# Optimization experiments

Measured on AMD Instinct MI355X. Metric: run time of the kernel, lower is better.

## Reference

```python
import jax, jax.numpy as jnp
import numpy as np

LEVEL_N = [81920, 20480, 5120, 1280, 320]  # faces at div..div-4 (div=6, 20*4^d)
K = 10  # SpherePHD conv kernel taps
W_SHAPES = [(64,3),(64,64),(128,64),(128,128),(256,128),(256,256),(256,256),(512,256),(512,512),(512,512),(512,512),(512,512),(512,512)]
BLOCKS = [[0,1],[2,3],[4,5,6],[7,8,9],[10,11,12]]  # conv indices per VGG block


def setup_inputs() -> dict:
    key = jax.random.key(0)
    ks = iter(jax.random.split(key, 64))
    d = {"x": jax.random.normal(next(ks), (2, 3, LEVEL_N[0]), jnp.float32)}
    for l, n in enumerate(LEVEL_N):
        d[f"conv_t{l}"] = jax.random.randint(next(ks), (n, K), 0, n, jnp.int32)
        d[f"adj_t{l}"] = jax.random.randint(next(ks), (n, 4), 0, n, jnp.int32)
        d[f"pool_t{l}"] = jax.random.randint(next(ks), (n // 4,), 0, n, jnp.int32)
    for i, (o, c) in enumerate(W_SHAPES):
        d[f"w{i}"] = jax.random.normal(next(ks), (o, c, K), jnp.float32) * (1.0 / np.sqrt(c * K))
        d[f"b{i}"] = jnp.zeros((o,), jnp.float32)
    return d


def phd_conv(x, w, b, table):
    # x: [B,C,N], table: [N,K] -> gather neighbors [B,C,N,K], weighted sum, ReLU
    g = x[:, :, table]
    y = jnp.einsum('bcnk,ock->bon', g, w) + b[None, :, None]
    return jax.nn.relu(y)


def phd_maxpool(x, adj, pool):
    # max over adjacent faces, then subsample to parent faces
    m = jnp.max(x[:, :, adj], axis=-1)  # [B,C,N]
    return m[:, :, pool]                # [B,C,N/4]


def reference(x, conv_t0, conv_t1, conv_t2, conv_t3, conv_t4,
              adj_t0, adj_t1, adj_t2, adj_t3, adj_t4,
              pool_t0, pool_t1, pool_t2, pool_t3, pool_t4,
              w0, w1, w2, w3, w4, w5, w6, w7, w8, w9, w10, w11, w12,
              b0, b1, b2, b3, b4, b5, b6, b7, b8, b9, b10, b11, b12):
    conv_ts = [conv_t0, conv_t1, conv_t2, conv_t3, conv_t4]
    adj_ts = [adj_t0, adj_t1, adj_t2, adj_t3, adj_t4]
    pool_ts = [pool_t0, pool_t1, pool_t2, pool_t3, pool_t4]
    ws = [w0, w1, w2, w3, w4, w5, w6, w7, w8, w9, w10, w11, w12]
    bs = [b0, b1, b2, b3, b4, b5, b6, b7, b8, b9, b10, b11, b12]
    h = x
    for lvl, idxs in enumerate(BLOCKS):
        for i in idxs:
            h = phd_conv(h, ws[i], bs[i], conv_ts[lvl])
        h = phd_maxpool(h, adj_ts[lvl], pool_ts[lvl])
    return h  # [2, 512, 80]
```

## Files before the change

### kernel.cpp

```cpp
#include <hip/hip_runtime.h>
#include <stdint.h>

typedef __bf16 bf16;
typedef bf16 bf16x8 __attribute__((ext_vector_type(8)));
typedef float f32x4 __attribute__((ext_vector_type(4)));
typedef unsigned short u16x8 __attribute__((ext_vector_type(8)));

__device__ __forceinline__ void gload_lds16(const bf16* g, bf16* l) {
    __builtin_amdgcn_global_load_lds(
        (const __attribute__((address_space(1))) void*)g,
        (__attribute__((address_space(3))) void*)l, 16, 0, 0);
}

struct PrepArgs {
    const float* src[12];
    int base[12];
    int dstoff[12];
    int Clog[12];
    int OT[12];
    int nClog[12];
};

__global__ __launch_bounds__(256) void prep_frag(PrepArgs a, bf16* __restrict__ dst)
{
    __shared__ bf16 lds[16 * 648];
    int bid = blockIdx.x;
    int l = 0;
#pragma unroll
    for (int i = 1; i < 12; i++) if (bid >= a.base[i]) l = i;
    int local = bid - a.base[l];
    int nClog = a.nClog[l];
    int cchunk = local & ((1 << nClog) - 1);
    int ot = local >> nClog;
    int Clog = a.Clog[l];
    int CK10 = 10 << Clog;
    const float* src = a.src[l];
    int t = threadIdx.x;

    size_t sbase = (size_t)(ot * 16) * CK10 + (size_t)cchunk * 640;
#pragma unroll
    for (int it = 0; it < 10; it++) {
        int idx = t + it * 256;
        int m = idx / 160;
        int i4 = idx - m * 160;
        float4 v = *(const float4*)(src + sbase + (size_t)m * CK10 + i4 * 4);
        bf16 b4[4] = {(bf16)v.x, (bf16)v.y, (bf16)v.z, (bf16)v.w};
        *(ushort4*)(&lds[m * 648 + i4 * 4]) = *(ushort4*)b4;
    }
    __syncthreads();

    int sub = t >> 6, ll = t & 63;
    int m = ll & 15, q = ll >> 4;
    int OTl = a.OT[l];
    size_t dbase = (size_t)a.dstoff[l];
#pragma unroll
    for (int tt = 0; tt < 5; tt++) {
        int tile = sub + tt * 4;
        int k = tile >> 1, half = tile & 1;
        int k32 = (k << (Clog - 5)) + cchunk * 2 + half;
        bf16 tmp[8];
#pragma unroll
        for (int j = 0; j < 8; j++)
            tmp[j] = lds[m * 648 + (half * 32 + q * 8 + j) * 10 + k];
        *(bf16x8*)(dst + dbase + ((size_t)(k32 * OTl + ot) << 9) + ll * 8) =
            *(bf16x8*)tmp;
    }
}

__global__ __launch_bounds__(256) void conv0_kernel(
    const float* __restrict__ x, const float* __restrict__ w0,
    const float* __restrict__ b0, const int* __restrict__ table,
    bf16* __restrict__ out)
{
    const int N = 81920;
    __shared__ float wls[30][64];
    __shared__ float bls[64];
    int tid = threadIdx.x;
    for (int i = tid; i < 1920; i += 256) {
        int o = i / 30, ck = i - o * 30;
        wls[ck][o] = w0[i];
    }
    if (tid < 64) bls[tid] = b0[tid];
    __syncthreads();

    int p = blockIdx.x * 256 + tid;
    int b = p >= N;
    int n = p - b * N;
    int idx[10];
    const int* trow = table + n * 10;
#pragma unroll
    for (int k = 0; k < 10; k++) idx[k] = trow[k];
    float xv[30];
#pragma unroll
    for (int c = 0; c < 3; c++)
#pragma unroll
        for (int k = 0; k < 10; k++)
            xv[c * 10 + k] = x[(b * 3 + c) * N + idx[k]];

    float acc[64];
#pragma unroll
    for (int o = 0; o < 64; o++) acc[o] = bls[o];
    for (int ck = 0; ck < 30; ck++) {
        float xs = xv[ck];
        const f32x4* wrow = (const f32x4*)(&wls[ck][0]);
#pragma unroll
        for (int o4 = 0; o4 < 16; o4++) {
            f32x4 w4 = wrow[o4];
            acc[o4 * 4 + 0] += xs * w4[0];
            acc[o4 * 4 + 1] += xs * w4[1];
            acc[o4 * 4 + 2] += xs * w4[2];
            acc[o4 * 4 + 3] += xs * w4[3];
        }
    }
    bf16x8 ob[8];
#pragma unroll
    for (int i = 0; i < 8; i++)
#pragma unroll
        for (int e = 0; e < 8; e++)
            ob[i][e] = (bf16)fmaxf(acc[i * 8 + e], 0.0f);
    bf16x8* dst = (bf16x8*)(out + (size_t)p * 64);
#pragma unroll
    for (int i = 0; i < 8; i++) dst[i] = ob[i];
}

template<int C, int TO, int TP>
__global__ __launch_bounds__(256) void conv_f(
    const bf16* __restrict__ in, const bf16* __restrict__ wfrag,
    const float* __restrict__ bias, const int* __restrict__ table,
    bf16* __restrict__ out, float* __restrict__ slab,
    int N, int O, int S, int PO)
{
    constexpr int BP = TP * 32;
    constexpr int CH = C / 64;
    constexpr int CHUNKS = CH * 10;
    constexpr int NW = 2 * TO + TP;
    constexpr int IMM = NW | 0x70 | 0xF00;
    __shared__ bf16 Xs[3][BP][64];
    __shared__ int rowoff[BP][10];

    const int tid = threadIdx.x;
    const int lane = tid & 63;
    const int wid = tid >> 6;
    const int wo = wid & 1, wp = wid >> 1;
    const int l16 = lane & 15, q = lane >> 4;

    const int p0 = blockIdx.x * BP;
    const int o0 = blockIdx.y * (TO * 32);
    const int z = blockIdx.z;
    const int OT = O >> 4;

    for (int j = tid; j < BP * 10; j += 256) {
        int pp = j / 10, k = j - pp * 10;
        int p = p0 + pp;
        int b = p >= N;
        int n = p - b * N;
        rowoff[pp][k] = (b * N + table[n * 10 + k]) * C;
    }
    __syncthreads();

    const int lrow = lane >> 3;
    const int gs = (lane & 7) ^ lrow;
    int srow[TP];
#pragma unroll
    for (int t = 0; t < TP; t++) srow[t] = wid * (TP * 8) + t * 8 + lrow;

    const int obase = (o0 >> 4) + wo * TO;

    const int per = CHUNKS / S;
    const int ck0 = z * per;

    auto stage = [&](int chunk, int b3) {
        int k = chunk / CH;
        int cofs = (chunk & (CH - 1)) * 64;
#pragma unroll
        for (int t = 0; t < TP; t++)
            gload_lds16(in + rowoff[srow[t]][k] + cofs + gs * 8,
                        &Xs[b3][wid * (TP * 8) + t * 8][0]);
    };
    auto loadW = [&](int chunk, bf16x8* dstA) {
        int k32b = chunk * 2;
#pragma unroll
        for (int ks = 0; ks < 2; ks++)
#pragma unroll
            for (int to = 0; to < TO; to++)
                dstA[ks * TO + to] = *(const bf16x8*)(
                    wfrag + (((size_t)(k32b + ks) * OT + obase + to) << 9) + lane * 8);
    };

    f32x4 acc[TO][TP];
#pragma unroll
    for (int a = 0; a < TO; a++)
#pragma unroll
        for (int c = 0; c < TP; c++) acc[a][c] = (f32x4){0.f, 0.f, 0.f, 0.f};

    bf16x8 wrA[2 * TO], wrB[2 * TO];

    stage(ck0, 0);
    loadW(ck0, wrA);
    stage(ck0 + 1, 1);

    const int browb = wp * (TP * 16);
    const int sx = l16 & 7;

    auto iter = [&](int j, bf16x8* cur, bf16x8* nxt, int bi, int bs) {
        __builtin_amdgcn_s_waitcnt(IMM);
        __builtin_amdgcn_s_barrier();
        __builtin_amdgcn_sched_barrier(0);
        int wc = j + 1 < per ? j + 1 : per - 1;
        loadW(ck0 + wc, nxt);
        int xc = j + 2 < per ? j + 2 : per - 1;
        stage(ck0 + xc, bs);
        __builtin_amdgcn_sched_barrier(0);
        const bf16* xb = &Xs[bi][0][0];
#pragma unroll
        for (int ks = 0; ks < 2; ks++) {
            int slot = ((ks * 4 + q) ^ sx) * 8;
            bf16x8 bfr[TP];
#pragma unroll
            for (int tp = 0; tp < TP; tp++)
                bfr[tp] = *(const bf16x8*)(xb + (browb + tp * 16 + l16) * 64 + slot);
#pragma unroll
            for (int to = 0; to < TO; to++)
#pragma unroll
                for (int tp = 0; tp < TP; tp++)
                    acc[to][tp] = __builtin_amdgcn_mfma_f32_16x16x32_bf16(
                        cur[ks * TO + to], bfr[tp], acc[to][tp], 0, 0, 0);
        }
    };

    int bi = 0, bs = 2;
    for (int j = 0; j < per; j += 2) {
        iter(j, wrA, wrB, bi, bs);
        bi = bi == 2 ? 0 : bi + 1; bs = bs == 2 ? 0 : bs + 1;
        iter(j + 1, wrB, wrA, bi, bs);
        bi = bi == 2 ? 0 : bi + 1; bs = bs == 2 ? 0 : bs + 1;
    }

    if (S == 1) {
#pragma unroll
        for (int to = 0; to < TO; ++to) {
            int ob = o0 + wo * (TO * 16) + to * 16 + q * 4;
            f32x4 bv = *(const f32x4*)(bias + ob);
#pragma unroll
            for (int tp = 0; tp < TP; ++tp) {
                int p = p0 + browb + tp * 16 + l16;
                union { ushort4 u4; unsigned short s[4]; } pk;
#pragma unroll
                for (int r = 0; r < 4; r++) {
                    float v = fmaxf(acc[to][tp][r] + bv[r], 0.0f);
                    union { bf16 h; unsigned short u; } cc;
                    cc.h = (bf16)v;
                    pk.s[r] = cc.u;
                }
                *(ushort4*)(out + (size_t)p * O + ob) = pk.u4;
            }
        }
    } else {
        float* sb = slab + (size_t)z * PO;
#pragma unroll
        for (int to = 0; to < TO; ++to) {
            int ob = o0 + wo * (TO * 16) + to * 16 + q * 4;
#pragma unroll
            for (int tp = 0; tp < TP; ++tp) {
                int p = p0 + browb + tp * 16 + l16;
                __builtin_nontemporal_store(acc[to][tp],
                    (f32x4*)(sb + (size_t)p * O + ob));
            }
        }
    }
}

__global__ __launch_bounds__(256) void epi_reduce(
    const float* __restrict__ slab, const float* __restrict__ bias,
    bf16* __restrict__ out, int PO, int Omask, int S)
{
    int t4 = (blockIdx.x * 256 + threadIdx.x) * 4;
    if (t4 >= PO) return;
    f32x4 s = __builtin_nontemporal_load((const f32x4*)(slab + t4));
    for (int zz = 1; zz < S; zz++)
        s += __builtin_nontemporal_load((const f32x4*)(slab + (size_t)zz * PO + t4));
    int o = t4 & Omask;
    f32x4 bv = *(const f32x4*)(bias + o);
    union { ushort4 u4; unsigned short e[4]; } pk;
#pragma unroll
    for (int r = 0; r < 4; r++) {
        float v = fmaxf(s[r] + bv[r], 0.0f);
        union { bf16 h; unsigned short u; } cc;
        cc.h = (bf16)v;
        pk.e[r] = cc.u;
    }
    *(ushort4*)((unsigned short*)out + t4) = pk.u4;
}

__global__ __launch_bounds__(256) void pool_kernel(
    const bf16* __restrict__ in, const int* __restrict__ adj,
    const int* __restrict__ pool, bf16* __restrict__ out,
    int N, int M, int c8shift)
{
    int t = blockIdx.x * 256 + threadIdx.x;
    int total = M << c8shift;
    if (t >= total) return;
    int cc = t & ((1 << c8shift) - 1);
    int j = t >> c8shift;
    int b = blockIdx.y;
    int C = 8 << c8shift;
    int s = pool[j];
    const int* a = adj + s * 4;
    const unsigned short* inu = (const unsigned short*)in;
    size_t base = (size_t)b * N * C + (size_t)cc * 8;
    u16x8 m = *(const u16x8*)(inu + base + (size_t)a[0] * C);
#pragma unroll
    for (int i = 1; i < 4; i++) {
        u16x8 v = *(const u16x8*)(inu + base + (size_t)a[i] * C);
#pragma unroll
        for (int e = 0; e < 8; e++) m[e] = v[e] > m[e] ? v[e] : m[e];
    }
    *(u16x8*)((unsigned short*)out + ((size_t)b * M + j) * C + (size_t)cc * 8) = m;
}

__global__ __launch_bounds__(256) void final_pool(
    const bf16* __restrict__ in, const int* __restrict__ adj,
    const int* __restrict__ pool, float* __restrict__ out)
{
    int t = blockIdx.x * 256 + threadIdx.x;
    if (t >= 81920) return;
    int j = t % 80;
    int rest = t / 80;
    int c = rest & 511;
    int b = rest >> 9;
    int s = pool[j];
    const int* a = adj + s * 4;
    float m = 0.0f;
#pragma unroll
    for (int i = 0; i < 4; i++) {
        float v = (float)in[((size_t)b * 320 + a[i]) * 512 + c];
        m = fmaxf(m, v);
    }
    out[t] = m;
}

extern "C" void kernel_launch(void* const* d_in, const int* in_sizes, int n_in,
                              void* d_out, int out_size, void* d_ws, size_t ws_size,
                              hipStream_t stream)
{
    const float* x = (const float*)d_in[0];
    const int* convT[5]; const int* adjT[5]; const int* poolT[5];
    for (int l = 0; l < 5; l++) {
        convT[l] = (const int*)d_in[1 + 3 * l];
        adjT[l]  = (const int*)d_in[2 + 3 * l];
        poolT[l] = (const int*)d_in[3 + 3 * l];
    }
    const float* W[13]; const float* Bs[13];
    for (int i = 0; i < 13; i++) {
        W[i]  = (const float*)d_in[16 + 2 * i];
        Bs[i] = (const float*)d_in[17 + 2 * i];
    }

    bf16* wbf = (bf16*)d_ws;
    bf16* A  = (bf16*)((char*)d_ws + (size_t)16343040 * 2);
    bf16* Bb = A + 10485760;
    float* slab = (float*)((char*)(Bb + 10485760));

    static const int woff[13] = {0, 0, 40960, 122880, 286720, 614400, 1269760,
                                 1925120, 3235840, 5857280, 8478720, 11100160, 13721600};

    PrepArgs pa;
    {
        static const int clog[12]  = {6,6,7,7,8,8,8,9,9,9,9,9};
        static const int otl[12]   = {4,8,8,16,16,16,32,32,32,32,32,32};
        static const int nclog[12] = {0,0,1,1,2,2,2,3,3,3,3,3};
        static const int basev[12] = {0,4,12,28,60,124,188,316,572,828,1084,1340};
        for (int i = 0; i < 12; i++) {
            pa.src[i] = W[i + 1];
            pa.base[i] = basev[i];
            pa.dstoff[i] = woff[i + 1];
            pa.Clog[i] = clog[i];
            pa.OT[i] = otl[i];
            pa.nClog[i] = nclog[i];
        }
    }
    prep_frag<<<dim3(1596), dim3(256), 0, stream>>>(pa, wbf);

    conv0_kernel<<<dim3(640), dim3(256), 0, stream>>>(x, W[0], Bs[0], convT[0], A);

    const int PO2 = 10240 * 256;
    const int PO3 = 2560 * 512;
    const int PO4 = 640 * 512;

    conv_f<64,2,4><<<dim3(1280, 1, 1), dim3(256), 0, stream>>>(A, wbf + woff[1], Bs[1], convT[0], Bb, slab, 81920, 64, 1, 0);
    pool_kernel<<<dim3(640, 2), dim3(256), 0, stream>>>(Bb, adjT[0], poolT[0], A, 81920, 20480, 3);
    conv_f<64,4,4><<<dim3(320, 1, 1), dim3(256), 0, stream>>>(A, wbf + woff[2], Bs[2], convT[1], Bb, slab, 20480, 128, 1, 0);
    conv_f<128,4,4><<<dim3(320, 1, 1), dim3(256), 0, stream>>>(Bb, wbf + woff[3], Bs[3], convT[1], A, slab, 20480, 128, 1, 0);
    pool_kernel<<<dim3(320, 2), dim3(256), 0, stream>>>(A, adjT[1], poolT[1], Bb, 20480, 5120, 4);
    conv_f<128,4,4><<<dim3(80, 2, 2), dim3(256), 0, stream>>>(Bb, wbf + woff[4], Bs[4], convT[2], A, slab, 5120, 256, 2, PO2);
    epi_reduce<<<dim3(PO2 / 1024), dim3(256), 0, stream>>>(slab, Bs[4], A, PO2, 255, 2);
    conv_f<256,4,4><<<dim3(80, 2, 2), dim3(256), 0, stream>>>(A, wbf + woff[5], Bs[5], convT[2], Bb, slab, 5120, 256, 2, PO2);
    epi_reduce<<<dim3(PO2 / 1024), dim3(256), 0, stream>>>(slab, Bs[5], Bb, PO2, 255, 2);
    conv_f<256,4,4><<<dim3(80, 2, 2), dim3(256), 0, stream>>>(Bb, wbf + woff[6], Bs[6], convT[2], A, slab, 5120, 256, 2, PO2);
    epi_reduce<<<dim3(PO2 / 1024), dim3(256), 0, stream>>>(slab, Bs[6], A, PO2, 255, 2);
    pool_kernel<<<dim3(160, 2), dim3(256), 0, stream>>>(A, adjT[2], poolT[2], Bb, 5120, 1280, 5);
    conv_f<256,4,4><<<dim3(20, 4, 4), dim3(256), 0, stream>>>(Bb, wbf + woff[7], Bs[7], convT[3], A, slab, 1280, 512, 4, PO3);
    epi_reduce<<<dim3(PO3 / 1024), dim3(256), 0, stream>>>(slab, Bs[7], A, PO3, 511, 4);
    conv_f<512,4,4><<<dim3(20, 4, 4), dim3(256), 0, stream>>>(A, wbf + woff[8], Bs[8], convT[3], Bb, slab, 1280, 512, 4, PO3);
    epi_reduce<<<dim3(PO3 / 1024), dim3(256), 0, stream>>>(slab, Bs[8], Bb, PO3, 511, 4);
    conv_f<512,4,4><<<dim3(20, 4, 4), dim3(256), 0, stream>>>(Bb, wbf + woff[9], Bs[9], convT[3], A, slab, 1280, 512, 4, PO3);
    epi_reduce<<<dim3(PO3 / 1024), dim3(256), 0, stream>>>(slab, Bs[9], A, PO3, 511, 4);
    pool_kernel<<<dim3(80, 2), dim3(256), 0, stream>>>(A, adjT[3], poolT[3], Bb, 1280, 320, 6);
    conv_f<512,2,4><<<dim3(5, 8, 8), dim3(256), 0, stream>>>(Bb, wbf + woff[10], Bs[10], convT[4], A, slab, 320, 512, 8, PO4);
    epi_reduce<<<dim3(PO4 / 1024), dim3(256), 0, stream>>>(slab, Bs[10], A, PO4, 511, 8);
    conv_f<512,2,4><<<dim3(5, 8, 8), dim3(256), 0, stream>>>(A, wbf + woff[11], Bs[11], convT[4], Bb, slab, 320, 512, 8, PO4);
    epi_reduce<<<dim3(PO4 / 1024), dim3(256), 0, stream>>>(slab, Bs[11], Bb, PO4, 511, 8);
    conv_f<512,2,4><<<dim3(5, 8, 8), dim3(256), 0, stream>>>(Bb, wbf + woff[12], Bs[12], convT[4], A, slab, 320, 512, 8, PO4);
    epi_reduce<<<dim3(PO4 / 1024), dim3(256), 0, stream>>>(slab, Bs[12], A, PO4, 511, 8);

    final_pool<<<dim3(320), dim3(256), 0, stream>>>(A, adjT[4], poolT[4], (float*)d_out);
}
```

Before: 598.8 us.

## Flatten conv grids with XCD-aware block remapping and retune tiles and split-K

Launches every conv_f as a 1D grid and decodes block coordinates in-kernel through several modes that group blocks by (blockIdx & 7), matching MI355X's round-robin dispatch across XCDs so blocks on one XCD share input rows or weight tiles in L2. It also shrinks the output tile (TO 4->2), drops split-K on the 256-channel level so its epi_reduce passes go away, and halves split-K on the 512-channel level. The aim is better L2 locality and more even occupancy, at the cost of extra integer index math and more blocks, each with less work.

```diff
diff --git a/kernel.cpp b/kernel.cpp
--- a/kernel.cpp
+++ b/kernel.cpp
@@ -128,7 +128,7 @@
     const bf16* __restrict__ in, const bf16* __restrict__ wfrag,
     const float* __restrict__ bias, const int* __restrict__ table,
     bf16* __restrict__ out, float* __restrict__ slab,
-    int N, int O, int S, int PO)
+    int N, int O, int S, int PO, int gx, int gy, int mode)
 {
     constexpr int BP = TP * 32;
     constexpr int CH = C / 64;
@@ -138,15 +138,32 @@
     __shared__ bf16 Xs[3][BP][64];
     __shared__ int rowoff[BP][10];
 
+    int B = blockIdx.x;
+    int bx, by, bz;
+    if (mode == 0) {
+        bx = B % gx; int r = B / gx; by = r % gy; bz = r / gy;
+    } else {
+        int c = B & 7, j = B >> 3;
+        if (mode == 1) {
+            int batch = c >> 2; by = c & 3; bz = 0;
+            bx = batch * (gx >> 1) + j;
+        } else if (mode == 2) {
+            int batch = c >> 2; by = (c >> 1) & 1; int xp = c & 1;
+            bx = batch * (gx >> 1) + j * 2 + xp; bz = 0;
+        } else {
+            by = c; bx = j % gx; bz = j / gx;
+        }
+    }
+
     const int tid = threadIdx.x;
     const int lane = tid & 63;
     const int wid = tid >> 6;
     const int wo = wid & 1, wp = wid >> 1;
     const int l16 = lane & 15, q = lane >> 4;
 
-    const int p0 = blockIdx.x * BP;
-    const int o0 = blockIdx.y * (TO * 32);
-    const int z = blockIdx.z;
+    const int p0 = bx * BP;
+    const int o0 = by * (TO * 32);
+    const int z = bz;
     const int OT = O >> 4;
 
     for (int j = tid; j < BP * 10; j += 256) {
@@ -383,34 +400,30 @@
 
     conv0_kernel<<<dim3(640), dim3(256), 0, stream>>>(x, W[0], Bs[0], convT[0], A);
 
-    const int PO2 = 10240 * 256;
     const int PO3 = 2560 * 512;
     const int PO4 = 640 * 512;
 
-    conv_f<64,2,4><<<dim3(1280, 1, 1), dim3(256), 0, stream>>>(A, wbf + woff[1], Bs[1], convT[0], Bb, slab, 81920, 64, 1, 0);
+    conv_f<64,2,4><<<dim3(1280), dim3(256), 0, stream>>>(A, wbf + woff[1], Bs[1], convT[0], Bb, slab, 81920, 64, 1, 0, 1280, 1, 0);
     pool_kernel<<<dim3(640, 2), dim3(256), 0, stream>>>(Bb, adjT[0], poolT[0], A, 81920, 20480, 3);
-    conv_f<64,4,4><<<dim3(320, 1, 1), dim3(256), 0, stream>>>(A, wbf + woff[2], Bs[2], convT[1], Bb, slab, 20480, 128, 1, 0);
-    conv_f<128,4,4><<<dim3(320, 1, 1), dim3(256), 0, stream>>>(Bb, wbf + woff[3], Bs[3], convT[1], A, slab, 20480, 128, 1, 0);
+    conv_f<64,2,4><<<dim3(640), dim3(256), 0, stream>>>(A, wbf + woff[2], Bs[2], convT[1], Bb, slab, 20480, 128, 1, 0, 320, 2, 2);
+    conv_f<128,2,4><<<dim3(640), dim3(256), 0, stream>>>(Bb, wbf + woff[3], Bs[3], convT[1], A, slab, 20480, 128, 1, 0, 320, 2, 2);
     pool_kernel<<<dim3(320, 2), dim3(256), 0, stream>>>(A, adjT[1], poolT[1], Bb, 20480, 5120, 4);
-    conv_f<128,4,4><<<dim3(80, 2, 2), dim3(256), 0, stream>>>(Bb, wbf + woff[4], Bs[4], convT[2], A, slab, 5120, 256, 2, PO2);
-    epi_reduce<<<dim3(PO2 / 1024), dim3(256), 0, stream>>>(slab, Bs[4], A, PO2, 255, 2);
-    conv_f<256,4,4><<<dim3(80, 2, 2), dim3(256), 0, stream>>>(A, wbf + woff[5], Bs[5], convT[2], Bb, slab, 5120, 256, 2, PO2);
-    epi_reduce<<<dim3(PO2 / 1024), dim3(256), 0, stream>>>(slab, Bs[5], Bb, PO2, 255, 2);
-    conv_f<256,4,4><<<dim3(80, 2, 2), dim3(256), 0, stream>>>(Bb, wbf + woff[6], Bs[6], convT[2], A, slab, 5120, 256, 2, PO2);
-    epi_reduce<<<dim3(PO2 / 1024), dim3(256), 0, stream>>>(slab, Bs[6], A, PO2, 255, 2);
+    conv_f<128,2,4><<<dim3(320), dim3(256), 0, stream>>>(Bb, wbf + woff[4], Bs[4], convT[2], A, slab, 5120, 256, 1, 0, 80, 4, 1);
+    conv_f<256,2,4><<<dim3(320), dim3(256), 0, stream>>>(A, wbf + woff[5], Bs[5], convT[2], Bb, slab, 5120, 256, 1, 0, 80, 4, 1);
+    conv_f<256,2,4><<<dim3(320), dim3(256), 0, stream>>>(Bb, wbf + woff[6], Bs[6], convT[2], A, slab, 5120, 256, 1, 0, 80, 4, 1);
     pool_kernel<<<dim3(160, 2), dim3(256), 0, stream>>>(A, adjT[2], poolT[2], Bb, 5120, 1280, 5);
-    conv_f<256,4,4><<<dim3(20, 4, 4), dim3(256), 0, stream>>>(Bb, wbf + woff[7], Bs[7], convT[3], A, slab, 1280, 512, 4, PO3);
-    epi_reduce<<<dim3(PO3 / 1024), dim3(256), 0, stream>>>(slab, Bs[7], A, PO3, 511, 4);
-    conv_f<512,4,4><<<dim3(20, 4, 4), dim3(256), 0, stream>>>(A, wbf + woff[8], Bs[8], convT[3], Bb, slab, 1280, 512, 4, PO3);
-    epi_reduce<<<dim3(PO3 / 1024), dim3(256), 0, stream>>>(slab, Bs[8], Bb, PO3, 511, 4);
-    conv_f<512,4,4><<<dim3(20, 4, 4), dim3(256), 0, stream>>>(Bb, wbf + woff[9], Bs[9], convT[3], A, slab, 1280, 512, 4, PO3);
-    epi_reduce<<<dim3(PO3 / 1024), dim3(256), 0, stream>>>(slab, Bs[9], A, PO3, 511, 4);
+    conv_f<256,2,4><<<dim3(320), dim3(256), 0, stream>>>(Bb, wbf + woff[7], Bs[7], convT[3], nullptr, slab, 1280, 512, 2, PO3, 20, 8, 3);
+    epi_reduce<<<dim3(PO3 / 1024), dim3(256), 0, stream>>>(slab, Bs[7], A, PO3, 511, 2);
+    conv_f<512,2,4><<<dim3(320), dim3(256), 0, stream>>>(A, wbf + woff[8], Bs[8], convT[3], nullptr, slab, 1280, 512, 2, PO3, 20, 8, 3);
+    epi_reduce<<<dim3(PO3 / 1024), dim3(256), 0, stream>>>(slab, Bs[8], Bb, PO3, 511, 2);
+    conv_f<512,2,4><<<dim3(320), dim3(256), 0, stream>>>(Bb, wbf + woff[9], Bs[9], convT[3], nullptr, slab, 1280, 512, 2, PO3, 20, 8, 3);
+    epi_reduce<<<dim3(PO3 / 1024), dim3(256), 0, stream>>>(slab, Bs[9], A, PO3, 511, 2);
     pool_kernel<<<dim3(80, 2), dim3(256), 0, stream>>>(A, adjT[3], poolT[3], Bb, 1280, 320, 6);
-    conv_f<512,2,4><<<dim3(5, 8, 8), dim3(256), 0, stream>>>(Bb, wbf + woff[10], Bs[10], convT[4], A, slab, 320, 512, 8, PO4);
+    conv_f<512,2,4><<<dim3(320), dim3(256), 0, stream>>>(Bb, wbf + woff[10], Bs[10], convT[4], nullptr, slab, 320, 512, 8, PO4, 5, 8, 3);
     epi_reduce<<<dim3(PO4 / 1024), dim3(256), 0, stream>>>(slab, Bs[10], A, PO4, 511, 8);
-    conv_f<512,2,4><<<dim3(5, 8, 8), dim3(256), 0, stream>>>(A, wbf + woff[11], Bs[11], convT[4], Bb, slab, 320, 512, 8, PO4);
+    conv_f<512,2,4><<<dim3(320), dim3(256), 0, stream>>>(A, wbf + woff[11], Bs[11], convT[4], nullptr, slab, 320, 512, 8, PO4, 5, 8, 3);
     epi_reduce<<<dim3(PO4 / 1024), dim3(256), 0, stream>>>(slab, Bs[11], Bb, PO4, 511, 8);
-    conv_f<512,2,4><<<dim3(5, 8, 8), dim3(256), 0, stream>>>(Bb, wbf + woff[12], Bs[12], convT[4], A, slab, 320, 512, 8, PO4);
+    conv_f<512,2,4><<<dim3(320), dim3(256), 0, stream>>>(Bb, wbf + woff[12], Bs[12], convT[4], nullptr, slab, 320, 512, 8, PO4, 5, 8, 3);
     epi_reduce<<<dim3(PO4 / 1024), dim3(256), 0, stream>>>(slab, Bs[12], A, PO4, 511, 8);
 
     final_pool<<<dim3(320), dim3(256), 0, stream>>>(A, adjT[4], poolT[4], (float*)d_out);
```

New measurement: 611.9 us. 1.02x slower.
